# Performance work log

Measured on AMD Instinct MI355X. Metric: run time of the kernel, lower is better.

The kernel has to match this reference:

```python
import jax, jax.numpy as jnp
import numpy as np

B, T, D, H = 8, 1024, 512, 8
D4 = 4 * D
SIGMA = 16.0
EPS = 1e-5


def layer_norm(x, w, b):
    m = jnp.mean(x, axis=-1, keepdims=True)
    v = jnp.mean((x - m) ** 2, axis=-1, keepdims=True)
    return (x - m) * jax.lax.rsqrt(v + EPS) * w + b


def setup_inputs() -> dict:
    key = jax.random.key(0)
    ks = jax.random.split(key, 12)
    return {
        "x": jax.random.normal(ks[0], (B, T, D), jnp.float32),
        "posv": jax.random.randint(ks[1], (B, T), 0, 64, jnp.int32),
        "posh": jax.random.randint(ks[2], (B, T), 0, 64, jnp.int32),
        "norm1_w": jnp.ones((D,), jnp.float32),
        "norm1_b": jnp.zeros((D,), jnp.float32),
        "in_w": jax.random.normal(ks[3], (3 * D, D), jnp.float32) * (D ** -0.5),
        "in_b": jnp.zeros((3 * D,), jnp.float32),
        "out_w": jax.random.normal(ks[4], (D, D), jnp.float32) * (D ** -0.5),
        "out_b": jnp.zeros((D,), jnp.float32),
        "norm2_w": jnp.ones((D,), jnp.float32),
        "norm2_b": jnp.zeros((D,), jnp.float32),
        "w1": jax.random.normal(ks[5], (D4, D), jnp.float32) * (D ** -0.5),
        "b1": jnp.zeros((D4,), jnp.float32),
        "w2": jax.random.normal(ks[6], (D, D4), jnp.float32) * (D4 ** -0.5),
        "b2": jnp.zeros((D,), jnp.float32),
        "gate": jnp.array(0.0, jnp.float32),
    }


def reference(x, posv, posh, norm1_w, norm1_b, in_w, in_b, out_w, out_b,
              norm2_w, norm2_b, w1, b1, w2, b2, gate):
    hd = D // H
    residual = x
    xn = layer_norm(x, norm1_w, norm1_b)

    # --- standard multi-head self-attention (dropout=eval identity) ---
    qkv = xn @ in_w.T + in_b                       # [B,T,3D]
    q, k, v = jnp.split(qkv, 3, axis=-1)
    q = q.reshape(B, T, H, hd).transpose(0, 2, 1, 3)  # [B,H,T,hd]
    k = k.reshape(B, T, H, hd).transpose(0, 2, 1, 3)
    v = v.reshape(B, T, H, hd).transpose(0, 2, 1, 3)
    scores = jnp.einsum("bhqd,bhkd->bhqk", q, k) * (hd ** -0.5)
    attn = jax.nn.softmax(scores, axis=-1)
    ctx = jnp.einsum("bhqk,bhkd->bhqd", attn, v)   # [B,H,T,hd]
    ctx = ctx.transpose(0, 2, 1, 3).reshape(B, T, D)
    std_out = ctx @ out_w.T + out_b

    # --- Gaussian kernel position attention ---
    pos = jnp.stack([posv, posh], axis=-1).astype(jnp.float32)  # [B,T,2]
    dist_sq = jnp.sum((pos[:, :, None, :] - pos[:, None, :, :]) ** 2, axis=-1)  # [B,T,T]
    kw = jnp.exp(-dist_sq / (2.0 * SIGMA ** 2))
    kw = kw / jnp.sum(kw, axis=-1, keepdims=True)
    kernel_out = kw @ xn                            # [B,T,D]

    g = jax.nn.sigmoid(gate)
    x1 = residual + g * std_out + (1.0 - g) * kernel_out

    # --- MLP block ---
    xn2 = layer_norm(x1, norm2_w, norm2_b)
    h = jax.nn.gelu(xn2 @ w1.T + b1, approximate=False)
    return x1 + h @ w2.T + b2
```

## Files before the change

kernel.cpp:

```cpp
#include <hip/hip_runtime.h>
#include <hip/hip_bf16.h>
#include <math.h>

typedef unsigned short ushort_t;
typedef short short8 __attribute__((ext_vector_type(8)));
typedef float f32x4 __attribute__((ext_vector_type(4)));

__device__ __forceinline__ float b2f(ushort_t u) {
  union { unsigned u; float f; } v; v.u = ((unsigned)u) << 16; return v.f;
}
__device__ __forceinline__ ushort_t f2b(float f) {
  union { float f; unsigned u; } v; v.f = f;
  unsigned r = (v.u + 0x7FFFu + ((v.u >> 16) & 1u)) >> 16;
  return (ushort_t)r;
}
__device__ __forceinline__ float gelu_fast(float v) {
  float u = 0.7978845608f * (v + 0.044715f * v * v * v);
  float a = fabsf(u);
  float t = exp2f(a * -2.8853900817779268f);
  float th = (1.f - t) / (1.f + t);
  th = copysignf(th, u);
  return 0.5f * v * (1.f + th);
}

union U16x8 { uint4 v; ushort_t s[8]; };

typedef const __attribute__((address_space(1))) unsigned int glb_u32;
typedef __attribute__((address_space(3))) unsigned int lds_u32;
__device__ __forceinline__ void gl_lds16(const ushort_t* g, ushort_t* l) {
  __builtin_amdgcn_global_load_lds((glb_u32*)g, (lds_u32*)l, 16, 0, 0);
}

__global__ __launch_bounds__(256) void prep_kernel(const float* __restrict__ s0,
                                                   const float* __restrict__ s1,
                                                   const float* __restrict__ s2,
                                                   const float* __restrict__ s3,
                                                   ushort_t* __restrict__ d0,
                                                   ushort_t* __restrict__ d1,
                                                   ushort_t* __restrict__ d2,
                                                   ushort_t* __restrict__ d3,
                                                   const float* __restrict__ x,
                                                   const float* __restrict__ w,
                                                   const float* __restrict__ b,
                                                   ushort_t* __restrict__ xnout,
                                                   const int* __restrict__ posv,
                                                   const int* __restrict__ posh,
                                                   ushort_t* __restrict__ kw) {
  int bid = blockIdx.x;
  int tid = threadIdx.x;
  if (bid < 3072) {
    long i = (long)bid * 256 + tid;
    const float* s; ushort_t* d; long off;
    if (i < 196608)       { s = s0; d = d0; off = i; }
    else if (i < 262144)  { s = s1; d = d1; off = i - 196608; }
    else if (i < 524288)  { s = s2; d = d2; off = i - 262144; }
    else                  { s = s3; d = d3; off = i - 524288; }
    float4 f = *(const float4*)(s + off * 4);
    union { uint2 v; ushort_t s[4]; } o;
    o.s[0] = f2b(f.x); o.s[1] = f2b(f.y); o.s[2] = f2b(f.z); o.s[3] = f2b(f.w);
    *(uint2*)(d + off * 4) = o.v;
  } else if (bid < 5120) {
    int wave = tid >> 6, lane = tid & 63;
    long token = (long)(bid - 3072) * 4 + wave;
    const float* xr = x + token * 512 + lane * 8;
    float4 a0 = *(const float4*)xr;
    float4 a1 = *(const float4*)(xr + 4);
    float xf[8] = {a0.x, a0.y, a0.z, a0.w, a1.x, a1.y, a1.z, a1.w};
    float s = 0.f, sq = 0.f;
#pragma unroll
    for (int i = 0; i < 8; i++) { s += xf[i]; sq += xf[i] * xf[i]; }
#pragma unroll
    for (int off = 1; off < 64; off <<= 1) { s += __shfl_xor(s, off); sq += __shfl_xor(sq, off); }
    float m = s * (1.f / 512.f);
    float var = sq * (1.f / 512.f) - m * m;
    float rs = rsqrtf(var + 1e-5f);
    float4 w0 = *(const float4*)(w + lane * 8);
    float4 w1v = *(const float4*)(w + lane * 8 + 4);
    float4 b0 = *(const float4*)(b + lane * 8);
    float4 b1v = *(const float4*)(b + lane * 8 + 4);
    float wf[8] = {w0.x, w0.y, w0.z, w0.w, w1v.x, w1v.y, w1v.z, w1v.w};
    float bf[8] = {b0.x, b0.y, b0.z, b0.w, b1v.x, b1v.y, b1v.z, b1v.w};
    U16x8 o;
#pragma unroll
    for (int i = 0; i < 8; i++) o.s[i] = f2b((xf[i] - m) * rs * wf[i] + bf[i]);
    *(uint4*)(xnout + token * 512 + lane * 8) = o.v;
  } else {
    int bb = bid - 5120;
    int bz = bb >> 10, i = bb & 1023;
    const int* pv = posv + bz * 1024;
    const int* ph = posh + bz * 1024;
    int pvi = pv[i], phi = ph[i];
    int j0 = tid * 4;
    int4 vj = *(const int4*)(pv + j0);
    int4 hj = *(const int4*)(ph + j0);
    int vv[4] = {vj.x, vj.y, vj.z, vj.w};
    int hh[4] = {hj.x, hj.y, hj.z, hj.w};
    float e[4]; float loc = 0.f;
#pragma unroll
    for (int u = 0; u < 4; u++) {
      int dv = pvi - vv[u], dh = phi - hh[u];
      e[u] = expf((float)(dv * dv + dh * dh) * (-1.f / 512.f));
      loc += e[u];
    }
#pragma unroll
    for (int off = 1; off < 64; off <<= 1) loc += __shfl_xor(loc, off);
    __shared__ float wsum[4];
    __shared__ float tot;
    if ((tid & 63) == 0) wsum[tid >> 6] = loc;
    __syncthreads();
    if (tid == 0) tot = wsum[0] + wsum[1] + wsum[2] + wsum[3];
    __syncthreads();
    float inv = 1.f / tot;
    union { uint2 v; ushort_t s[4]; } o;
#pragma unroll
    for (int u = 0; u < 4; u++) o.s[u] = f2b(e[u] * inv);
    *(uint2*)&kw[((long)(bz * 1024 + i)) * 1024 + j0] = o.v;
  }
}

__global__ __launch_bounds__(256) void ln_b_kernel(const ushort_t* __restrict__ x,
                                                   const float* __restrict__ w,
                                                   const float* __restrict__ b,
                                                   ushort_t* __restrict__ out) {
  int tid = threadIdx.x, wave = tid >> 6, lane = tid & 63;
  long token = (long)blockIdx.x * 4 + wave;
  U16x8 ux; ux.v = *(const uint4*)(x + token * 512 + lane * 8);
  float xf[8], s = 0.f, sq = 0.f;
#pragma unroll
  for (int i = 0; i < 8; i++) { xf[i] = b2f(ux.s[i]); s += xf[i]; sq += xf[i] * xf[i]; }
#pragma unroll
  for (int off = 1; off < 64; off <<= 1) { s += __shfl_xor(s, off); sq += __shfl_xor(sq, off); }
  float m = s * (1.f / 512.f);
  float var = sq * (1.f / 512.f) - m * m;
  float rs = rsqrtf(var + 1e-5f);
  float4 w0 = *(const float4*)(w + lane * 8);
  float4 w1v = *(const float4*)(w + lane * 8 + 4);
  float4 b0 = *(const float4*)(b + lane * 8);
  float4 b1v = *(const float4*)(b + lane * 8 + 4);
  float wf[8] = {w0.x, w0.y, w0.z, w0.w, w1v.x, w1v.y, w1v.z, w1v.w};
  float bf[8] = {b0.x, b0.y, b0.z, b0.w, b1v.x, b1v.y, b1v.z, b1v.w};
  U16x8 o;
#pragma unroll
  for (int i = 0; i < 8; i++) o.s[i] = f2b((xf[i] - m) * rs * wf[i] + bf[i]);
  *(uint4*)(out + token * 512 + lane * 8) = o.v;
}

__global__ __launch_bounds__(256) void tr_kernel(const ushort_t* __restrict__ in,
                                                 ushort_t* __restrict__ out,
                                                 int R, int C) {
  __shared__ ushort_t tile[64 * 64];
  int z = blockIdx.z, r0 = blockIdx.y * 64, c0 = blockIdx.x * 64;
  const ushort_t* src = in + (long)z * R * C;
  ushort_t* dst = out + (long)z * R * C;
  int tid = threadIdx.x;
  int tr = tid >> 2;
  const ushort_t* s = src + (long)(r0 + tr) * C + c0;
  int g = (tr + (tr >> 4)) & 7;
#pragma unroll
  for (int u = 0; u < 2; u++) {
    int c = (tid & 3) + u * 4;
    *(uint4*)&tile[tr * 64 + (c ^ g) * 8] = *(const uint4*)(s + c * 8);
  }
  __syncthreads();
  int oc = tid >> 2, ob = (tid & 3) * 16;
  U16x8 o0, o1;
#pragma unroll
  for (int j = 0; j < 16; j++) {
    int r = ob + j;
    int gg = (r + (r >> 4)) & 7;
    ushort_t val = tile[r * 64 + (((oc >> 3) ^ gg)) * 8 + (oc & 7)];
    if (j < 8) o0.s[j] = val; else o1.s[j - 8] = val;
  }
  ushort_t* d = dst + (long)(c0 + oc) * R + r0 + ob;
  *(uint4*)d = o0.v;
  *(uint4*)(d + 8) = o1.v;
}

struct GemmP {
  const ushort_t* A; const ushort_t* Bm;
  long sA, sB, sC;
  int lda, ldb, ldc, K;
  const float* biasf;
  const float* residf;
  const ushort_t* auxb;
  float* outf;
  ushort_t* outb;
  ushort_t* qp; ushort_t* kp; ushort_t* vp;
  const float* gate;
};

template <int BM, int BN, int EPI>
__global__ __launch_bounds__(256) void gemm_k(GemmP p) {
  constexpr int TI = BM / 32, TJ = BN / 32;
  constexpr int RA = BM / 64, RB = BN / 64;
  __shared__ ushort_t As[4][BM * 32];
  __shared__ ushort_t Bs[4][BN * 32];
  int tid = threadIdx.x, wv = tid >> 6, lane = tid & 63;
  int quad = lane >> 4, l15 = lane & 15;
  int bl = blockIdx.x + gridDim.x * blockIdx.y;
  int m0 = (bl % gridDim.y) * BM;
  int n0 = (bl / gridDim.y) * BN;
  int z = blockIdx.z;
  const ushort_t* A = p.A + (long)z * p.sA;
  const ushort_t* Bm = p.Bm + (long)z * p.sB;
  int wm = (wv & 1) * (BM / 2), wn = (wv >> 1) * (BN / 2);
  f32x4 acc[TI][TJ];
#pragma unroll
  for (int i = 0; i < TI; i++)
#pragma unroll
    for (int j = 0; j < TJ; j++)
#pragma unroll
      for (int r = 0; r < 4; r++) acc[i][j][r] = 0.f;

  int srow = tid >> 2;
  int sc = ((tid & 3) ^ ((tid >> 3) & 3)) * 8;
  const ushort_t* ga = A + (long)(m0 + srow) * p.lda + sc;
  const ushort_t* gb = Bm + (long)(n0 + srow) * p.ldb + sc;
  long a64 = (long)64 * p.lda, b64 = (long)64 * p.ldb;
  int aswz = (quad ^ ((l15 >> 1) & 3)) * 8;
  int nsteps = p.K >> 5;

#pragma unroll
  for (int s = 0; s < 2; s++) {
#pragma unroll
    for (int rr = 0; rr < RA; rr++)
      gl_lds16(ga + s * 32 + rr * a64, As[s] + rr * 2048 + wv * 512);
#pragma unroll
    for (int rr = 0; rr < RB; rr++)
      gl_lds16(gb + s * 32 + rr * b64, Bs[s] + rr * 2048 + wv * 512);
  }

  for (int ks = 0; ks < nsteps; ks += 2) {
    asm volatile("s_waitcnt vmcnt(0)" ::: "memory");
    __builtin_amdgcn_s_barrier();
    if (ks + 2 < nsteps) {
#pragma unroll
      for (int s = 0; s < 2; s++) {
        int st = ks + 2 + s, bf = st & 3;
        const ushort_t* a0 = ga + st * 32;
        const ushort_t* b0 = gb + st * 32;
#pragma unroll
        for (int rr = 0; rr < RA; rr++)
          gl_lds16(a0 + rr * a64, As[bf] + rr * 2048 + wv * 512);
#pragma unroll
        for (int rr = 0; rr < RB; rr++)
          gl_lds16(b0 + rr * b64, Bs[bf] + rr * 2048 + wv * 512);
      }
    }
#pragma unroll
    for (int hs = 0; hs < 2; hs++) {
      int cur = (ks + hs) & 3;
      short8 av[TI], bv[TJ];
#pragma unroll
      for (int ti = 0; ti < TI; ti++)
        av[ti] = *(const short8*)&As[cur][(wm + ti * 16 + l15) * 32 + aswz];
#pragma unroll
      for (int tj = 0; tj < TJ; tj++)
        bv[tj] = *(const short8*)&Bs[cur][(wn + tj * 16 + l15) * 32 + aswz];
#pragma unroll
      for (int ti = 0; ti < TI; ti++)
#pragma unroll
        for (int tj = 0; tj < TJ; tj++)
          acc[ti][tj] = __builtin_amdgcn_mfma_f32_16x16x32_bf16(av[ti], bv[tj], acc[ti][tj], 0, 0, 0);
    }
  }

  float g = 0.f;
  if constexpr (EPI == 2) g = 1.f / (1.f + expf(-p.gate[0]));
#pragma unroll
  for (int ti = 0; ti < TI; ti++) {
#pragma unroll
    for (int tj = 0; tj < TJ; tj++) {
#pragma unroll
      for (int r = 0; r < 4; r++) {
        int gm = m0 + wm + ti * 16 + quad * 4 + r;
        int n = n0 + wn + tj * 16 + l15;
        float v = acc[ti][tj][r];
        if constexpr (EPI == 1) {
          p.outb[(long)z * p.sC + (long)gm * p.ldc + n] = f2b(v);
        } else if constexpr (EPI == 2) {
          v += p.biasf[n];
          long idx = (long)gm * 512 + n;
          p.outb[idx] = f2b(p.residf[idx] + g * v + (1.f - g) * b2f(p.auxb[idx]));
        } else {
          v += p.biasf[n];
          long idx = (long)gm * 512 + n;
          p.outf[idx] = v + b2f(p.auxb[idx]);
        }
      }
    }
  }
}

template <int EPI, int LDA, int LDB, int K, int LDC>
__global__ __launch_bounds__(256) void wgemm_k(GemmP p) {
  constexpr int NSTEPS = K / 32;
  constexpr long A16 = 16L * LDA, B16 = 16L * LDB;
  __shared__ __align__(16) ushort_t lds[4][4096];
  int tid = threadIdx.x, wv = tid >> 6, lane = tid & 63;
  int quad = lane >> 4, l15 = lane & 15;
  int m0 = blockIdx.x * 64;
  int n0 = (blockIdx.y * 4 + wv) * 64;
  ushort_t* Aw = lds[wv];
  ushort_t* Bw = lds[wv] + 2048;
  const ushort_t* ga = p.A + (long)(m0 + (lane >> 2)) * LDA + (lane & 3) * 8;
  const ushort_t* gb = p.Bm + (long)(n0 + (lane >> 2)) * LDB + (lane & 3) * 8;

  f32x4 acc[4][4];
#pragma unroll
  for (int i = 0; i < 4; i++)
#pragma unroll
    for (int j = 0; j < 4; j++)
#pragma unroll
      for (int r = 0; r < 4; r++) acc[i][j][r] = 0.f;

#define WSTAGE(T)                                                \
  {                                                              \
    const ushort_t* a0 = ga + (T) * 32;                          \
    const ushort_t* b0 = gb + (T) * 32;                          \
    _Pragma("unroll")                                            \
    for (int c = 0; c < 4; c++) gl_lds16(a0 + c * A16, Aw + c * 512); \
    _Pragma("unroll")                                            \
    for (int c = 0; c < 4; c++) gl_lds16(b0 + c * B16, Bw + c * 512); \
  }

  WSTAGE(0);
  for (int t = 0; t < NSTEPS; t++) {
    asm volatile("s_waitcnt vmcnt(0)" ::: "memory");
    short8 av[4], bv[4];
#pragma unroll
    for (int i = 0; i < 4; i++) {
      av[i] = *(const short8*)&Aw[(i * 16 + l15) * 32 + quad * 8];
      bv[i] = *(const short8*)&Bw[(i * 16 + l15) * 32 + quad * 8];
    }
    asm volatile("s_waitcnt lgkmcnt(0)" ::: "memory");
    __builtin_amdgcn_sched_barrier(0);
    if (t + 1 < NSTEPS) WSTAGE(t + 1);
    __builtin_amdgcn_s_setprio(1);
#pragma unroll
    for (int i = 0; i < 4; i++)
#pragma unroll
      for (int j = 0; j < 4; j++)
        acc[i][j] = __builtin_amdgcn_mfma_f32_16x16x32_bf16(av[i], bv[j], acc[i][j], 0, 0, 0);
    __builtin_amdgcn_s_setprio(0);
  }
#undef WSTAGE

#pragma unroll
  for (int ti = 0; ti < 4; ti++) {
#pragma unroll
    for (int tj = 0; tj < 4; tj++) {
#pragma unroll
      for (int r = 0; r < 4; r++) {
        int gm = m0 + ti * 16 + quad * 4 + r;
        int n = n0 + tj * 16 + l15;
        float v = acc[ti][tj][r];
        if constexpr (EPI == 0) {
          v += p.biasf[n];
          int bb = gm >> 10, tt = gm & 1023;
          if (n < 512) {
            int h = n >> 6, d = n & 63;
            p.qp[((long)(bb * 8 + h) * 1024 + tt) * 64 + d] = f2b(v * 0.18033688011112042f);
          } else if (n < 1024) {
            int n2 = n - 512, h = n2 >> 6, d = n2 & 63;
            p.kp[((long)(bb * 8 + h) * 1024 + tt) * 64 + d] = f2b(v);
          } else {
            int n2 = n - 1024, h = n2 >> 6, d = n2 & 63;
            p.vp[((long)(bb * 8 + h) * 1024 + tt) * 64 + d] = f2b(v);
          }
        } else {
          v += p.biasf[n];
          p.outb[(long)gm * LDC + n] = f2b(gelu_fast(v));
        }
      }
    }
  }
}

__global__ __launch_bounds__(256) void flash_k(const ushort_t* __restrict__ q,
                                               const ushort_t* __restrict__ k,
                                               const ushort_t* __restrict__ vT,
                                               ushort_t* __restrict__ ctx) {
  int bl = blockIdx.x + gridDim.x * blockIdx.y;
  int bh = bl % 64;
  int q0 = (bl / 64) * 128;
  int tid = threadIdx.x, wv = tid >> 6, lane = tid & 63;
  int quad = lane >> 4, l15 = lane & 15;
  __shared__ ushort_t Ks[2][64 * 64], Vt[2][64 * 64];
  __shared__ ushort_t Pt[128 * 64];
  int wm = wv * 32;

  short8 qf[2][2];
#pragma unroll
  for (int tq = 0; tq < 2; tq++)
#pragma unroll
    for (int kk = 0; kk < 2; kk++)
      qf[tq][kk] = *(const short8*)&q[((long)bh * 1024 + q0 + wm + tq * 16 + l15) * 64 + kk * 32 + quad * 8];

  int srow = tid >> 3;
  int sc = ((tid & 7) ^ ((tid >> 3) & 7)) * 8;
#pragma unroll
  for (int e = 0; e < 2; e++) {
    gl_lds16(&k[((long)bh * 1024 + e * 32 + srow) * 64 + sc], Ks[0] + e * 2048 + wv * 512);
    gl_lds16(&vT[((long)bh * 64 + e * 32 + srow) * 1024 + sc], Vt[0] + e * 2048 + wv * 512);
  }

  f32x4 O[2][4];
#pragma unroll
  for (int tq = 0; tq < 2; tq++)
#pragma unroll
    for (int td = 0; td < 4; td++)
#pragma unroll
      for (int r = 0; r < 4; r++) O[tq][td][r] = 0.f;
  float ls[2] = {0.f, 0.f};

  int pswz = (l15 & 7) << 1;
  for (int kt = 0; kt < 16; kt++) {
    int cur = kt & 1;
    asm volatile("s_waitcnt vmcnt(0)" ::: "memory");
    __builtin_amdgcn_s_barrier();
    if (kt + 1 < 16) {
#pragma unroll
      for (int e = 0; e < 2; e++) {
        gl_lds16(&k[((long)bh * 1024 + (kt + 1) * 64 + e * 32 + srow) * 64 + sc], Ks[cur ^ 1] + e * 2048 + wv * 512);
        gl_lds16(&vT[((long)bh * 64 + e * 32 + srow) * 1024 + (kt + 1) * 64 + sc], Vt[cur ^ 1] + e * 2048 + wv * 512);
      }
    }
#pragma unroll
    for (int tq = 0; tq < 2; tq++) {
      f32x4 S[4];
#pragma unroll
      for (int tk = 0; tk < 4; tk++) {
#pragma unroll
        for (int r = 0; r < 4; r++) S[tk][r] = 0.f;
#pragma unroll
        for (int kk = 0; kk < 2; kk++) {
          short8 kf = *(const short8*)&Ks[cur][(tk * 16 + l15) * 64 + ((kk * 4 + quad) ^ (l15 & 7)) * 8];
          S[tk] = __builtin_amdgcn_mfma_f32_16x16x32_bf16(kf, qf[tq][kk], S[tk], 0, 0, 0);
        }
      }
#pragma unroll
      for (int tk = 0; tk < 4; tk++) {
        float p0 = exp2f(S[tk][0]);
        float p1 = exp2f(S[tk][1]);
        float p2 = exp2f(S[tk][2]);
        float p3 = exp2f(S[tk][3]);
        ls[tq] += (p0 + p1) + (p2 + p3);
        unsigned lo = __builtin_amdgcn_perm(__float_as_uint(p1), __float_as_uint(p0), 0x07060302u);
        unsigned hi = __builtin_amdgcn_perm(__float_as_uint(p3), __float_as_uint(p2), 0x07060302u);
        int gnum = (tk * 4 + quad) ^ pswz;
        uint2 pr; pr.x = lo; pr.y = hi;
        *(uint2*)&Pt[(wm + tq * 16 + l15) * 64 + gnum * 4] = pr;
      }
    }
#pragma unroll
    for (int tq = 0; tq < 2; tq++) {
#pragma unroll
      for (int kk = 0; kk < 2; kk++) {
        short8 pf = *(const short8*)&Pt[(wm + tq * 16 + l15) * 64 + (((kk * 8 + quad * 2) ^ pswz)) * 4];
#pragma unroll
        for (int td = 0; td < 4; td++) {
          short8 vf = *(const short8*)&Vt[cur][(td * 16 + l15) * 64 + ((kk * 4 + quad) ^ (l15 & 7)) * 8];
          O[tq][td] = __builtin_amdgcn_mfma_f32_16x16x32_bf16(pf, vf, O[tq][td], 0, 0, 0);
        }
      }
    }
  }
#pragma unroll
  for (int tq = 0; tq < 2; tq++) {
    ls[tq] += __shfl_xor(ls[tq], 16);
    ls[tq] += __shfl_xor(ls[tq], 32);
  }
  int bb = bh >> 3, h = bh & 7;
#pragma unroll
  for (int tq = 0; tq < 2; tq++) {
#pragma unroll
    for (int r = 0; r < 4; r++) {
      int qrow = quad * 4 + r;
      float inv = 1.f / __shfl(ls[tq], (lane & 48) | qrow);
      long row = (long)bb * 1024 + q0 + wm + tq * 16 + qrow;
#pragma unroll
      for (int td = 0; td < 4; td++)
        ctx[row * 512 + h * 64 + td * 16 + l15] = f2b(O[tq][td][r] * inv);
    }
  }
}

extern "C" void kernel_launch(void* const* d_in, const int* in_sizes, int n_in,
                              void* d_out, int out_size, void* d_ws, size_t ws_size,
                              hipStream_t stream) {
  const float* x    = (const float*)d_in[0];
  const int* posv   = (const int*)d_in[1];
  const int* posh   = (const int*)d_in[2];
  const float* n1w  = (const float*)d_in[3];
  const float* n1b  = (const float*)d_in[4];
  const float* in_w = (const float*)d_in[5];
  const float* in_b = (const float*)d_in[6];
  const float* outw = (const float*)d_in[7];
  const float* outb = (const float*)d_in[8];
  const float* n2w  = (const float*)d_in[9];
  const float* n2b  = (const float*)d_in[10];
  const float* w1   = (const float*)d_in[11];
  const float* b1   = (const float*)d_in[12];
  const float* w2   = (const float*)d_in[13];
  const float* b2   = (const float*)d_in[14];
  const float* gate = (const float*)d_in[15];
  float* out = (float*)d_out;

  char* ws = (char*)d_ws;
  const size_t MB = 1024 * 1024;
  ushort_t* q    = (ushort_t*)(ws + 0 * MB);
  ushort_t* kk   = (ushort_t*)(ws + 8 * MB);
  ushort_t* vtmp = (ushort_t*)(ws + 16 * MB);
  ushort_t* vT   = (ushort_t*)(ws + 24 * MB);
  ushort_t* kw   = (ushort_t*)(ws + 32 * MB);
  ushort_t* xn   = (ushort_t*)(ws + 48 * MB);
  ushort_t* xnT  = (ushort_t*)(ws + 56 * MB);
  ushort_t* ctx  = (ushort_t*)(ws + 64 * MB);
  ushort_t* ko   = (ushort_t*)(ws + 72 * MB);
  ushort_t* x1b  = (ushort_t*)(ws + 80 * MB);
  ushort_t* xn2  = (ushort_t*)(ws + 16 * MB);
  ushort_t* inwb = (ushort_t*)(ws + 96 * MB);
  ushort_t* owb  = (ushort_t*)(ws + 98 * MB);
  ushort_t* w1b  = (ushort_t*)(ws + 99 * MB);
  ushort_t* w2b  = (ushort_t*)(ws + 101 * MB);
  ushort_t* h    = (ushort_t*)(ws + 24 * MB);

  prep_kernel<<<13312, 256, 0, stream>>>(in_w, outw, w1, w2, inwb, owb, w1b, w2b,
                                         x, n1w, n1b, xn, posv, posh, kw);
  {
    GemmP p = {};
    p.A = xn; p.Bm = inwb;
    p.biasf = in_b; p.qp = q; p.kp = kk; p.vp = vtmp;
    wgemm_k<0, 512, 512, 512, 0><<<dim3(128, 6), 256, 0, stream>>>(p);
  }
  tr_kernel<<<dim3(1, 16, 64), 256, 0, stream>>>(vtmp, vT, 1024, 64);
  flash_k<<<dim3(8, 64, 1), 256, 0, stream>>>(q, kk, vT, ctx);
  tr_kernel<<<dim3(8, 16, 8), 256, 0, stream>>>(xn, xnT, 1024, 512);
  {
    GemmP p = {};
    p.A = kw; p.Bm = xnT; p.lda = 1024; p.ldb = 1024; p.ldc = 512; p.K = 1024;
    p.sA = 1024L * 1024; p.sB = 512L * 1024; p.sC = 1024L * 512;
    p.outb = ko;
    gemm_k<64, 128, 1><<<dim3(4, 16, 8), 256, 0, stream>>>(p);
  }
  {
    GemmP p = {};
    p.A = ctx; p.Bm = owb; p.lda = 512; p.ldb = 512; p.K = 512;
    p.biasf = outb; p.residf = x; p.auxb = ko; p.outb = x1b; p.gate = gate;
    gemm_k<64, 64, 2><<<dim3(8, 128, 1), 256, 0, stream>>>(p);
  }
  ln_b_kernel<<<2048, 256, 0, stream>>>(x1b, n2w, n2b, xn2);
  {
    GemmP p = {};
    p.A = xn2; p.Bm = w1b;
    p.biasf = b1; p.outb = h;
    wgemm_k<3, 512, 512, 512, 2048><<<dim3(128, 8), 256, 0, stream>>>(p);
  }
  {
    GemmP p = {};
    p.A = h; p.Bm = w2b; p.lda = 2048; p.ldb = 2048; p.K = 2048;
    p.biasf = b2; p.auxb = x1b; p.outf = out;
    gemm_k<64, 128, 4><<<dim3(4, 128, 1), 256, 0, stream>>>(p);
  }
}
```

Baseline: 290.3 us.

## Merge transposes and co-schedule flash attention with kernel-weight GEMM in one launch

Combines the two transpose launches into one kernel and merges flash attention with the Gaussian-kernel batched GEMM into a single launch that splits blocks by index. The aim is to cut launch count and let the two independent workloads fill the GPU together, avoiding a tail-underutilized flash launch. The QKV and MLP-up GEMMs move from the per-wave wgemm kernel to the shared-tile gemm_k template with new epilogues. Risks: the merged kernel has uneven block costs, and the wgemm-to-gemm_k swap could be slower.

Measured after the change: 266.6 us. -8.1%, faster.

```diff
diff --git a/kernel.cpp b/kernel.cpp
--- a/kernel.cpp
+++ b/kernel.cpp
@@ -145,13 +145,22 @@
   *(uint4*)(out + token * 512 + lane * 8) = o.v;
 }
 
-__global__ __launch_bounds__(256) void tr_kernel(const ushort_t* __restrict__ in,
-                                                 ushort_t* __restrict__ out,
-                                                 int R, int C) {
+__global__ __launch_bounds__(256) void tr2_kernel(const ushort_t* __restrict__ in0,
+                                                  ushort_t* __restrict__ out0,
+                                                  const ushort_t* __restrict__ in1,
+                                                  ushort_t* __restrict__ out1) {
   __shared__ ushort_t tile[64 * 64];
-  int z = blockIdx.z, r0 = blockIdx.y * 64, c0 = blockIdx.x * 64;
-  const ushort_t* src = in + (long)z * R * C;
-  ushort_t* dst = out + (long)z * R * C;
+  int b = blockIdx.x;
+  const ushort_t* src; ushort_t* dst; int C, r0, c0;
+  if (b < 1024) {
+    int z = b >> 4; r0 = (b & 15) * 64; c0 = 0; C = 64;
+    src = in0 + (long)z * 1024 * 64; dst = out0 + (long)z * 1024 * 64;
+  } else {
+    int bb = b - 1024;
+    int z = bb >> 7; r0 = ((bb >> 3) & 15) * 64; c0 = (bb & 7) * 64; C = 512;
+    src = in1 + (long)z * 1024 * 512; dst = out1 + (long)z * 1024 * 512;
+  }
+  int R = 1024;
   int tid = threadIdx.x;
   int tr = tid >> 2;
   const ushort_t* s = src + (long)(r0 + tr) * C + c0;
@@ -276,85 +285,6 @@
         int gm = m0 + wm + ti * 16 + quad * 4 + r;
         int n = n0 + wn + tj * 16 + l15;
         float v = acc[ti][tj][r];
-        if constexpr (EPI == 1) {
-          p.outb[(long)z * p.sC + (long)gm * p.ldc + n] = f2b(v);
-        } else if constexpr (EPI == 2) {
-          v += p.biasf[n];
-          long idx = (long)gm * 512 + n;
-          p.outb[idx] = f2b(p.residf[idx] + g * v + (1.f - g) * b2f(p.auxb[idx]));
-        } else {
-          v += p.biasf[n];
-          long idx = (long)gm * 512 + n;
-          p.outf[idx] = v + b2f(p.auxb[idx]);
-        }
-      }
-    }
-  }
-}
-
-template <int EPI, int LDA, int LDB, int K, int LDC>
-__global__ __launch_bounds__(256) void wgemm_k(GemmP p) {
-  constexpr int NSTEPS = K / 32;
-  constexpr long A16 = 16L * LDA, B16 = 16L * LDB;
-  __shared__ __align__(16) ushort_t lds[4][4096];
-  int tid = threadIdx.x, wv = tid >> 6, lane = tid & 63;
-  int quad = lane >> 4, l15 = lane & 15;
-  int m0 = blockIdx.x * 64;
-  int n0 = (blockIdx.y * 4 + wv) * 64;
-  ushort_t* Aw = lds[wv];
-  ushort_t* Bw = lds[wv] + 2048;
-  const ushort_t* ga = p.A + (long)(m0 + (lane >> 2)) * LDA + (lane & 3) * 8;
-  const ushort_t* gb = p.Bm + (long)(n0 + (lane >> 2)) * LDB + (lane & 3) * 8;
-
-  f32x4 acc[4][4];
-#pragma unroll
-  for (int i = 0; i < 4; i++)
-#pragma unroll
-    for (int j = 0; j < 4; j++)
-#pragma unroll
-      for (int r = 0; r < 4; r++) acc[i][j][r] = 0.f;
-
-#define WSTAGE(T)                                                \
-  {                                                              \
-    const ushort_t* a0 = ga + (T) * 32;                          \
-    const ushort_t* b0 = gb + (T) * 32;                          \
-    _Pragma("unroll")                                            \
-    for (int c = 0; c < 4; c++) gl_lds16(a0 + c * A16, Aw + c * 512); \
-    _Pragma("unroll")                                            \
-    for (int c = 0; c < 4; c++) gl_lds16(b0 + c * B16, Bw + c * 512); \
-  }
-
-  WSTAGE(0);
-  for (int t = 0; t < NSTEPS; t++) {
-    asm volatile("s_waitcnt vmcnt(0)" ::: "memory");
-    short8 av[4], bv[4];
-#pragma unroll
-    for (int i = 0; i < 4; i++) {
-      av[i] = *(const short8*)&Aw[(i * 16 + l15) * 32 + quad * 8];
-      bv[i] = *(const short8*)&Bw[(i * 16 + l15) * 32 + quad * 8];
-    }
-    asm volatile("s_waitcnt lgkmcnt(0)" ::: "memory");
-    __builtin_amdgcn_sched_barrier(0);
-    if (t + 1 < NSTEPS) WSTAGE(t + 1);
-    __builtin_amdgcn_s_setprio(1);
-#pragma unroll
-    for (int i = 0; i < 4; i++)
-#pragma unroll
-      for (int j = 0; j < 4; j++)
-        acc[i][j] = __builtin_amdgcn_mfma_f32_16x16x32_bf16(av[i], bv[j], acc[i][j], 0, 0, 0);
-    __builtin_amdgcn_s_setprio(0);
-  }
-#undef WSTAGE
-
-#pragma unroll
-  for (int ti = 0; ti < 4; ti++) {
-#pragma unroll
-    for (int tj = 0; tj < 4; tj++) {
-#pragma unroll
-      for (int r = 0; r < 4; r++) {
-        int gm = m0 + ti * 16 + quad * 4 + r;
-        int n = n0 + tj * 16 + l15;
-        float v = acc[ti][tj][r];
         if constexpr (EPI == 0) {
           v += p.biasf[n];
           int bb = gm >> 10, tt = gm & 1023;
@@ -368,120 +298,212 @@
             int n2 = n - 1024, h = n2 >> 6, d = n2 & 63;
             p.vp[((long)(bb * 8 + h) * 1024 + tt) * 64 + d] = f2b(v);
           }
+        } else if constexpr (EPI == 2) {
+          v += p.biasf[n];
+          long idx = (long)gm * 512 + n;
+          p.outb[idx] = f2b(p.residf[idx] + g * v + (1.f - g) * b2f(p.auxb[idx]));
+        } else if constexpr (EPI == 3) {
+          v += p.biasf[n];
+          p.outb[(long)gm * p.ldc + n] = f2b(gelu_fast(v));
         } else {
           v += p.biasf[n];
-          p.outb[(long)gm * LDC + n] = f2b(gelu_fast(v));
-        }
-      }
-    }
-  }
-}
-
-__global__ __launch_bounds__(256) void flash_k(const ushort_t* __restrict__ q,
-                                               const ushort_t* __restrict__ k,
-                                               const ushort_t* __restrict__ vT,
-                                               ushort_t* __restrict__ ctx) {
-  int bl = blockIdx.x + gridDim.x * blockIdx.y;
-  int bh = bl % 64;
-  int q0 = (bl / 64) * 128;
+          long idx = (long)gm * 512 + n;
+          p.outf[idx] = v + b2f(p.auxb[idx]);
+        }
+      }
+    }
+  }
+}
+
+__global__ __launch_bounds__(256) void fk_kernel(const ushort_t* __restrict__ q,
+                                                 const ushort_t* __restrict__ k,
+                                                 const ushort_t* __restrict__ vT,
+                                                 ushort_t* __restrict__ ctx,
+                                                 const ushort_t* __restrict__ kwp,
+                                                 const ushort_t* __restrict__ xnT,
+                                                 ushort_t* __restrict__ ko) {
+  __shared__ __align__(16) ushort_t smem[24576];
+  int b = blockIdx.x;
   int tid = threadIdx.x, wv = tid >> 6, lane = tid & 63;
   int quad = lane >> 4, l15 = lane & 15;
-  __shared__ ushort_t Ks[2][64 * 64], Vt[2][64 * 64];
-  __shared__ ushort_t Pt[128 * 64];
-  int wm = wv * 32;
-
-  short8 qf[2][2];
-#pragma unroll
-  for (int tq = 0; tq < 2; tq++)
-#pragma unroll
-    for (int kk = 0; kk < 2; kk++)
-      qf[tq][kk] = *(const short8*)&q[((long)bh * 1024 + q0 + wm + tq * 16 + l15) * 64 + kk * 32 + quad * 8];
-
-  int srow = tid >> 3;
-  int sc = ((tid & 7) ^ ((tid >> 3) & 7)) * 8;
-#pragma unroll
-  for (int e = 0; e < 2; e++) {
-    gl_lds16(&k[((long)bh * 1024 + e * 32 + srow) * 64 + sc], Ks[0] + e * 2048 + wv * 512);
-    gl_lds16(&vT[((long)bh * 64 + e * 32 + srow) * 1024 + sc], Vt[0] + e * 2048 + wv * 512);
-  }
-
-  f32x4 O[2][4];
-#pragma unroll
-  for (int tq = 0; tq < 2; tq++)
-#pragma unroll
-    for (int td = 0; td < 4; td++)
-#pragma unroll
-      for (int r = 0; r < 4; r++) O[tq][td][r] = 0.f;
-  float ls[2] = {0.f, 0.f};
-
-  int pswz = (l15 & 7) << 1;
-  for (int kt = 0; kt < 16; kt++) {
-    int cur = kt & 1;
-    asm volatile("s_waitcnt vmcnt(0)" ::: "memory");
-    __builtin_amdgcn_s_barrier();
-    if (kt + 1 < 16) {
-#pragma unroll
-      for (int e = 0; e < 2; e++) {
-        gl_lds16(&k[((long)bh * 1024 + (kt + 1) * 64 + e * 32 + srow) * 64 + sc], Ks[cur ^ 1] + e * 2048 + wv * 512);
-        gl_lds16(&vT[((long)bh * 64 + e * 32 + srow) * 1024 + (kt + 1) * 64 + sc], Vt[cur ^ 1] + e * 2048 + wv * 512);
+
+  if (b < 512) {
+    int bh = b & 63;
+    int q0 = (b >> 6) * 128;
+    ushort_t* Ksp = smem;
+    ushort_t* Vtp = smem + 8192;
+    ushort_t* Ptp = smem + 16384;
+    int wm = wv * 32;
+
+    short8 qf[2][2];
+#pragma unroll
+    for (int tq = 0; tq < 2; tq++)
+#pragma unroll
+      for (int kk2 = 0; kk2 < 2; kk2++)
+        qf[tq][kk2] = *(const short8*)&q[((long)bh * 1024 + q0 + wm + tq * 16 + l15) * 64 + kk2 * 32 + quad * 8];
+
+    int srow = tid >> 3;
+    int sc = ((tid & 7) ^ ((tid >> 3) & 7)) * 8;
+#pragma unroll
+    for (int e = 0; e < 2; e++) {
+      gl_lds16(&k[((long)bh * 1024 + e * 32 + srow) * 64 + sc], Ksp + e * 2048 + wv * 512);
+      gl_lds16(&vT[((long)bh * 64 + e * 32 + srow) * 1024 + sc], Vtp + e * 2048 + wv * 512);
+    }
+
+    f32x4 O[2][4];
+#pragma unroll
+    for (int tq = 0; tq < 2; tq++)
+#pragma unroll
+      for (int td = 0; td < 4; td++)
+#pragma unroll
+        for (int r = 0; r < 4; r++) O[tq][td][r] = 0.f;
+    float ls[2] = {0.f, 0.f};
+
+    int pswz = (l15 & 7) << 1;
+    for (int kt = 0; kt < 16; kt++) {
+      int cur = kt & 1;
+      asm volatile("s_waitcnt vmcnt(0)" ::: "memory");
+      __builtin_amdgcn_s_barrier();
+      if (kt + 1 < 16) {
+#pragma unroll
+        for (int e = 0; e < 2; e++) {
+          gl_lds16(&k[((long)bh * 1024 + (kt + 1) * 64 + e * 32 + srow) * 64 + sc], Ksp + (cur ^ 1) * 4096 + e * 2048 + wv * 512);
+          gl_lds16(&vT[((long)bh * 64 + e * 32 + srow) * 1024 + (kt + 1) * 64 + sc], Vtp + (cur ^ 1) * 4096 + e * 2048 + wv * 512);
+        }
+      }
+#pragma unroll
+      for (int tq = 0; tq < 2; tq++) {
+        f32x4 S[4];
+#pragma unroll
+        for (int tk = 0; tk < 4; tk++) {
+#pragma unroll
+          for (int r = 0; r < 4; r++) S[tk][r] = 0.f;
+#pragma unroll
+          for (int kk2 = 0; kk2 < 2; kk2++) {
+            short8 kf = *(const short8*)&Ksp[cur * 4096 + (tk * 16 + l15) * 64 + ((kk2 * 4 + quad) ^ (l15 & 7)) * 8];
+            S[tk] = __builtin_amdgcn_mfma_f32_16x16x32_bf16(kf, qf[tq][kk2], S[tk], 0, 0, 0);
+          }
+        }
+#pragma unroll
+        for (int tk = 0; tk < 4; tk++) {
+          float p0 = exp2f(S[tk][0]);
+          float p1 = exp2f(S[tk][1]);
+          float p2 = exp2f(S[tk][2]);
+          float p3 = exp2f(S[tk][3]);
+          ls[tq] += (p0 + p1) + (p2 + p3);
+          unsigned lo = __builtin_amdgcn_perm(__float_as_uint(p1), __float_as_uint(p0), 0x07060302u);
+          unsigned hi = __builtin_amdgcn_perm(__float_as_uint(p3), __float_as_uint(p2), 0x07060302u);
+          int gnum = (tk * 4 + quad) ^ pswz;
+          uint2 pr; pr.x = lo; pr.y = hi;
+          *(uint2*)&Ptp[(wm + tq * 16 + l15) * 64 + gnum * 4] = pr;
+        }
+      }
+#pragma unroll
+      for (int tq = 0; tq < 2; tq++) {
+#pragma unroll
+        for (int kk2 = 0; kk2 < 2; kk2++) {
+          short8 pf = *(const short8*)&Ptp[(wm + tq * 16 + l15) * 64 + (((kk2 * 8 + quad * 2) ^ pswz)) * 4];
+#pragma unroll
+          for (int td = 0; td < 4; td++) {
+            short8 vf = *(const short8*)&Vtp[cur * 4096 + (td * 16 + l15) * 64 + ((kk2 * 4 + quad) ^ (l15 & 7)) * 8];
+            O[tq][td] = __builtin_amdgcn_mfma_f32_16x16x32_bf16(pf, vf, O[tq][td], 0, 0, 0);
+          }
+        }
       }
     }
 #pragma unroll
     for (int tq = 0; tq < 2; tq++) {
-      f32x4 S[4];
-#pragma unroll
-      for (int tk = 0; tk < 4; tk++) {
-#pragma unroll
-        for (int r = 0; r < 4; r++) S[tk][r] = 0.f;
-#pragma unroll
-        for (int kk = 0; kk < 2; kk++) {
-          short8 kf = *(const short8*)&Ks[cur][(tk * 16 + l15) * 64 + ((kk * 4 + quad) ^ (l15 & 7)) * 8];
-          S[tk] = __builtin_amdgcn_mfma_f32_16x16x32_bf16(kf, qf[tq][kk], S[tk], 0, 0, 0);
-        }
-      }
-#pragma unroll
-      for (int tk = 0; tk < 4; tk++) {
-        float p0 = exp2f(S[tk][0]);
-        float p1 = exp2f(S[tk][1]);
-        float p2 = exp2f(S[tk][2]);
-        float p3 = exp2f(S[tk][3]);
-        ls[tq] += (p0 + p1) + (p2 + p3);
-        unsigned lo = __builtin_amdgcn_perm(__float_as_uint(p1), __float_as_uint(p0), 0x07060302u);
-        unsigned hi = __builtin_amdgcn_perm(__float_as_uint(p3), __float_as_uint(p2), 0x07060302u);
-        int gnum = (tk * 4 + quad) ^ pswz;
-        uint2 pr; pr.x = lo; pr.y = hi;
-        *(uint2*)&Pt[(wm + tq * 16 + l15) * 64 + gnum * 4] = pr;
-      }
-    }
+      ls[tq] += __shfl_xor(ls[tq], 16);
+      ls[tq] += __shfl_xor(ls[tq], 32);
+    }
+    int bb = bh >> 3, h = bh & 7;
 #pragma unroll
     for (int tq = 0; tq < 2; tq++) {
 #pragma unroll
-      for (int kk = 0; kk < 2; kk++) {
-        short8 pf = *(const short8*)&Pt[(wm + tq * 16 + l15) * 64 + (((kk * 8 + quad * 2) ^ pswz)) * 4];
-#pragma unroll
-        for (int td = 0; td < 4; td++) {
-          short8 vf = *(const short8*)&Vt[cur][(td * 16 + l15) * 64 + ((kk * 4 + quad) ^ (l15 & 7)) * 8];
-          O[tq][td] = __builtin_amdgcn_mfma_f32_16x16x32_bf16(pf, vf, O[tq][td], 0, 0, 0);
-        }
-      }
-    }
-  }
-#pragma unroll
-  for (int tq = 0; tq < 2; tq++) {
-    ls[tq] += __shfl_xor(ls[tq], 16);
-    ls[tq] += __shfl_xor(ls[tq], 32);
-  }
-  int bb = bh >> 3, h = bh & 7;
-#pragma unroll
-  for (int tq = 0; tq < 2; tq++) {
-#pragma unroll
-    for (int r = 0; r < 4; r++) {
-      int qrow = quad * 4 + r;
-      float inv = 1.f / __shfl(ls[tq], (lane & 48) | qrow);
-      long row = (long)bb * 1024 + q0 + wm + tq * 16 + qrow;
-#pragma unroll
-      for (int td = 0; td < 4; td++)
-        ctx[row * 512 + h * 64 + td * 16 + l15] = f2b(O[tq][td][r] * inv);
+      for (int r = 0; r < 4; r++) {
+        int qrow = quad * 4 + r;
+        float inv = 1.f / __shfl(ls[tq], (lane & 48) | qrow);
+        long row = (long)bb * 1024 + q0 + wm + tq * 16 + qrow;
+#pragma unroll
+        for (int td = 0; td < 4; td++)
+          ctx[row * 512 + h * 64 + td * 16 + l15] = f2b(O[tq][td][r] * inv);
+      }
+    }
+  } else {
+    int b2 = b - 512;
+    int z = b2 >> 6, bl = b2 & 63;
+    int m0 = (bl & 15) * 64;
+    int n0 = (bl >> 4) * 128;
+    const ushort_t* A = kwp + (long)z * (1024L * 1024);
+    const ushort_t* Bm = xnT + (long)z * (512L * 1024);
+    ushort_t* Asp = smem;
+    ushort_t* Bsp = smem + 8192;
+    int wm = (wv & 1) * 32, wn = (wv >> 1) * 64;
+    f32x4 acc[2][4];
+#pragma unroll
+    for (int i = 0; i < 2; i++)
+#pragma unroll
+      for (int j = 0; j < 4; j++)
+#pragma unroll
+        for (int r = 0; r < 4; r++) acc[i][j][r] = 0.f;
+
+    int srow = tid >> 2;
+    int sc = ((tid & 3) ^ ((tid >> 3) & 3)) * 8;
+    const ushort_t* ga = A + (long)(m0 + srow) * 1024 + sc;
+    const ushort_t* gb = Bm + (long)(n0 + srow) * 1024 + sc;
+    const long a64 = 64L * 1024, b64 = 64L * 1024;
+    int aswz = (quad ^ ((l15 >> 1) & 3)) * 8;
+
+#pragma unroll
+    for (int s = 0; s < 2; s++) {
+      gl_lds16(ga + s * 32, Asp + s * 2048 + wv * 512);
+#pragma unroll
+      for (int rr = 0; rr < 2; rr++)
+        gl_lds16(gb + s * 32 + rr * b64, Bsp + s * 4096 + rr * 2048 + wv * 512);
+    }
+
+    for (int ks = 0; ks < 32; ks += 2) {
+      asm volatile("s_waitcnt vmcnt(0)" ::: "memory");
+      __builtin_amdgcn_s_barrier();
+      if (ks + 2 < 32) {
+#pragma unroll
+        for (int s = 0; s < 2; s++) {
+          int st = ks + 2 + s, bf = st & 3;
+          gl_lds16(ga + st * 32, Asp + bf * 2048 + wv * 512);
+#pragma unroll
+          for (int rr = 0; rr < 2; rr++)
+            gl_lds16(gb + st * 32 + rr * b64, Bsp + bf * 4096 + rr * 2048 + wv * 512);
+        }
+      }
+#pragma unroll
+      for (int hs = 0; hs < 2; hs++) {
+        int cur = (ks + hs) & 3;
+        short8 av[2], bv[4];
+#pragma unroll
+        for (int ti = 0; ti < 2; ti++)
+          av[ti] = *(const short8*)&Asp[cur * 2048 + (wm + ti * 16 + l15) * 32 + aswz];
+#pragma unroll
+        for (int tj = 0; tj < 4; tj++)
+          bv[tj] = *(const short8*)&Bsp[cur * 4096 + (wn + tj * 16 + l15) * 32 + aswz];
+#pragma unroll
+        for (int ti = 0; ti < 2; ti++)
+#pragma unroll
+          for (int tj = 0; tj < 4; tj++)
+            acc[ti][tj] = __builtin_amdgcn_mfma_f32_16x16x32_bf16(av[ti], bv[tj], acc[ti][tj], 0, 0, 0);
+      }
+    }
+
+#pragma unroll
+    for (int ti = 0; ti < 2; ti++) {
+#pragma unroll
+      for (int tj = 0; tj < 4; tj++) {
+#pragma unroll
+        for (int r = 0; r < 4; r++) {
+          int gm = m0 + wm + ti * 16 + quad * 4 + r;
+          int n = n0 + wn + tj * 16 + l15;
+          ko[(long)z * (1024L * 512) + (long)gm * 512 + n] = f2b(acc[ti][tj][r]);
+        }
+      }
     }
   }
 }
@@ -530,20 +552,12 @@
                                          x, n1w, n1b, xn, posv, posh, kw);
   {
     GemmP p = {};
-    p.A = xn; p.Bm = inwb;
+    p.A = xn; p.Bm = inwb; p.lda = 512; p.ldb = 512; p.K = 512;
     p.biasf = in_b; p.qp = q; p.kp = kk; p.vp = vtmp;
-    wgemm_k<0, 512, 512, 512, 0><<<dim3(128, 6), 256, 0, stream>>>(p);
-  }
-  tr_kernel<<<dim3(1, 16, 64), 256, 0, stream>>>(vtmp, vT, 1024, 64);
-  flash_k<<<dim3(8, 64, 1), 256, 0, stream>>>(q, kk, vT, ctx);
-  tr_kernel<<<dim3(8, 16, 8), 256, 0, stream>>>(xn, xnT, 1024, 512);
-  {
-    GemmP p = {};
-    p.A = kw; p.Bm = xnT; p.lda = 1024; p.ldb = 1024; p.ldc = 512; p.K = 1024;
-    p.sA = 1024L * 1024; p.sB = 512L * 1024; p.sC = 1024L * 512;
-    p.outb = ko;
-    gemm_k<64, 128, 1><<<dim3(4, 16, 8), 256, 0, stream>>>(p);
-  }
+    gemm_k<64, 128, 0><<<dim3(12, 128, 1), 256, 0, stream>>>(p);
+  }
+  tr2_kernel<<<2048, 256, 0, stream>>>(vtmp, vT, xn, xnT);
+  fk_kernel<<<1024, 256, 0, stream>>>(q, kk, vT, ctx, kw, xnT, ko);
   {
     GemmP p = {};
     p.A = ctx; p.Bm = owb; p.lda = 512; p.ldb = 512; p.K = 512;
@@ -553,9 +567,9 @@
   ln_b_kernel<<<2048, 256, 0, stream>>>(x1b, n2w, n2b, xn2);
   {
     GemmP p = {};
-    p.A = xn2; p.Bm = w1b;
+    p.A = xn2; p.Bm = w1b; p.lda = 512; p.ldb = 512; p.ldc = 2048; p.K = 512;
     p.biasf = b1; p.outb = h;
-    wgemm_k<3, 512, 512, 512, 2048><<<dim3(128, 8), 256, 0, stream>>>(p);
+    gemm_k<64, 128, 3><<<dim3(16, 128, 1), 256, 0, stream>>>(p);
   }
   {
     GemmP p = {};
```
